# Optimization experiments

Measured on AMD Instinct MI355X. Metric: run time of the kernel, lower is better.

Reference implementation:

```python
import jax, jax.numpy as jnp
import numpy as np

D_MODEL = 768
NUM_HEADS = 12
D_K = D_MODEL // NUM_HEADS


def setup_inputs() -> dict:
    key = jax.random.key(0)
    ks = jax.random.split(key, 7)
    B, S = 4, 2048
    query = jax.random.normal(ks[0], (B, S, D_MODEL), dtype=jnp.float32)
    key_t = jax.random.normal(ks[1], (B, S, D_MODEL), dtype=jnp.float32)
    value = jax.random.normal(ks[2], (B, S, D_MODEL), dtype=jnp.float32)
    lim = 1.0 / np.sqrt(D_MODEL)
    Wq = jax.random.uniform(ks[3], (D_MODEL, D_MODEL), jnp.float32, -lim, lim)  # torch Linear weight [out,in]
    bq = jax.random.uniform(ks[4], (D_MODEL,), jnp.float32, -lim, lim)
    Wo = jax.random.uniform(ks[5], (D_MODEL, D_MODEL), jnp.float32, -lim, lim)
    bo = jax.random.uniform(ks[6], (D_MODEL,), jnp.float32, -lim, lim)
    return {"query": query, "key": key_t, "value": value,
            "Wq": Wq, "bq": bq, "Wo": Wo, "bo": bo}


def _proj_heads(x, W, b):
    # x: [B,S,D] -> [B,H,S,d_k]; torch Linear: x @ W.T + b
    B, S, _ = x.shape
    y = x @ W.T + b
    return y.reshape(B, S, NUM_HEADS, D_K).transpose(0, 2, 1, 3)


def reference(query, key, value, Wq, bq, Wo, bo):
    # Faithful to source: linear_q is used for q, k AND v (source bug).
    q = _proj_heads(query, Wq, bq)
    k = _proj_heads(key, Wq, bq)
    v = _proj_heads(value, Wq, bq)
    scale = 1.0 / jnp.sqrt(jnp.asarray(D_K, q.dtype))
    scores = jnp.einsum('bhqd,bhkd->bhqk', q, k) * scale  # [B,H,S,S]
    attn = jax.nn.softmax(scores, axis=-1)
    out = jnp.einsum('bhqk,bhkd->bhqd', attn, v)  # [B,H,S,d_k]
    B, H, S, dk = out.shape
    out = out.transpose(0, 2, 1, 3).reshape(B, S, H * dk)
    return out @ Wo.T + bo
```

## Files before the change

### kernel.cpp

```cpp
#include <hip/hip_runtime.h>
#include <math.h>

typedef _Float16 f16x8 __attribute__((ext_vector_type(8)));
typedef _Float16 f16x4 __attribute__((ext_vector_type(4)));
typedef float    f32x4 __attribute__((ext_vector_type(4)));
typedef unsigned short us4 __attribute__((ext_vector_type(4)));
typedef unsigned int u32;
typedef unsigned int u32x4 __attribute__((ext_vector_type(4)));

constexpr int DM = 768, NH = 12, DK = 64, SEQ = 2048, BB = 4;
constexpr int MROWS = BB * SEQ;
constexpr size_t XELE = (size_t)MROWS * DM;
constexpr size_t WELE = (size_t)DM * DM;

constexpr size_t OFF_X16  = 0;
constexpr size_t OFF_W16  = 3 * XELE;
constexpr size_t OFF_WO16 = OFF_W16 + WELE;
constexpr size_t OFF_QKV  = OFF_WO16 + WELE;
constexpr size_t OFF_ATT  = OFF_QKV + 3 * XELE;
constexpr size_t TOT_CVT  = OFF_QKV;


constexpr float QSCALE = 0.125f * 1.44269504f;
constexpr float MSEED = -8.0f;

__device__ __forceinline__ void gload16(const _Float16* g, _Float16* l) {
    __builtin_amdgcn_global_load_lds(
        (const __attribute__((address_space(1))) unsigned int*)g,
        (__attribute__((address_space(3))) unsigned int*)l, 16, 0, 0);
}

__device__ __forceinline__ uint2 pack4(float a, float b, float c, float d) {
    uint2 r;
    r.x = __builtin_bit_cast(u32, __builtin_amdgcn_cvt_pkrtz(a, b));
    r.y = __builtin_bit_cast(u32, __builtin_amdgcn_cvt_pkrtz(c, d));
    return r;
}

__global__ __launch_bounds__(256) void cvt_kernel(
    const float* __restrict__ q, const float* __restrict__ k,
    const float* __restrict__ v, const float* __restrict__ wq,
    const float* __restrict__ wo, _Float16* __restrict__ dst)
{
    const size_t i = ((size_t)blockIdx.x * 256 + threadIdx.x) * 4;
    if (i >= TOT_CVT) return;
    const float* src; size_t base;
    if      (i < XELE)            { src = q;  base = 0; }
    else if (i < 2 * XELE)        { src = k;  base = XELE; }
    else if (i < 3 * XELE)        { src = v;  base = 2 * XELE; }
    else if (i < OFF_WO16)        { src = wq; base = OFF_W16; }
    else                          { src = wo; base = OFF_WO16; }
    const float4 f = *(const float4*)(src + (i - base));
    _Float16 h4[4] = {(_Float16)f.x, (_Float16)f.y, (_Float16)f.z, (_Float16)f.w};
    *(us4*)(dst + i) = *(us4*)h4;
}

template <int MODE>
__global__ __launch_bounds__(256) void mfma_gemm(
    const _Float16* __restrict__ Xbase, const _Float16* __restrict__ Wmat,
    const float* __restrict__ bias, void* __restrict__ Yout)
{
    __shared__ _Float16 smem[(MODE == 0) ? 128 * 136 : 16384];

    const int bid = blockIdx.x;
    const int xs  = bid & 7;
    const int rr  = bid >> 3;
    const int m_blk = ((rr & 7) << 3) | xs;
    const int tt  = rr >> 3;
    const int n_blk = (MODE == 0) ? (tt % 6) : tt;
    const int z     = (MODE == 0) ? (tt / 6) : 0;

    const int tid  = threadIdx.x;
    const int w    = tid >> 6, lane = tid & 63;
    const int cl   = lane & 15;
    const int g    = lane >> 4;
    const int m0   = m_blk * 128, n0 = n_blk * 128;
    const _Float16* X = Xbase + (size_t)z * XELE;

    const int wr = w >> 1, wc = w & 1;
    const int lrow = lane >> 2;
    const int lcol = (lane & 3) * 8;

    f32x4 acc[4][4] = {};

    constexpr int NK = DM / 32;
#pragma unroll
    for (int t = 0; t < 2; ++t) {
        const int c = w + t * 4;
        gload16(X    + (size_t)(m0 + c * 16 + lrow) * DM + lcol, &smem[c * 512]);
        gload16(Wmat + (size_t)(n0 + c * 16 + lrow) * DM + lcol, &smem[4096 + c * 512]);
    }

    int cur = 0;
    for (int ki = 0; ki < NK; ++ki) {
        __syncthreads();
        if (ki + 1 < NK) {
            const int kn = (ki + 1) * 32;
            _Float16* dst = &smem[(cur ^ 1) * 8192];
#pragma unroll
            for (int t = 0; t < 2; ++t) {
                const int c = w + t * 4;
                gload16(X    + (size_t)(m0 + c * 16 + lrow) * DM + kn + lcol, &dst[c * 512]);
                gload16(Wmat + (size_t)(n0 + c * 16 + lrow) * DM + kn + lcol, &dst[4096 + c * 512]);
            }
        }
        const _Float16* As = &smem[cur * 8192];
        const _Float16* Bs = As + 4096;

        f16x8 a[4], bfr[4];
#pragma unroll
        for (int mt = 0; mt < 4; ++mt)
            a[mt] = *(const f16x8*)&As[(wr * 64 + mt * 16 + cl) * 32 + g * 8];
#pragma unroll
        for (int nt = 0; nt < 4; ++nt)
            bfr[nt] = *(const f16x8*)&Bs[(wc * 64 + nt * 16 + cl) * 32 + g * 8];
#pragma unroll
        for (int mt = 0; mt < 4; ++mt)
#pragma unroll
            for (int nt = 0; nt < 4; ++nt)
                acc[mt][nt] = __builtin_amdgcn_mfma_f32_16x16x32_f16(
                    a[mt], bfr[nt], acc[mt][nt], 0, 0, 0);
        cur ^= 1;
    }

    if (MODE == 1) {
#pragma unroll
        for (int nt = 0; nt < 4; ++nt) {
            const int col = n0 + wc * 64 + nt * 16 + cl;
            const float bv = bias[col];
#pragma unroll
            for (int mt = 0; mt < 4; ++mt)
#pragma unroll
                for (int r = 0; r < 4; ++r) {
                    const int row = m0 + wr * 64 + mt * 16 + g * 4 + r;
                    ((float*)Yout)[(size_t)row * DM + col] = acc[mt][nt][r] + bv;
                }
        }
        return;
    }

    __syncthreads();
    const float sc = (z == 0) ? QSCALE : 1.0f;
#pragma unroll
    for (int nt = 0; nt < 4; ++nt) {
        const int col = wc * 64 + nt * 16 + cl;
        const float bv = bias[n0 + col];
#pragma unroll
        for (int mt = 0; mt < 4; ++mt)
#pragma unroll
            for (int r = 0; r < 4; ++r) {
                const int row = wr * 64 + mt * 16 + g * 4 + r;
                const _Float16 hv = (_Float16)((acc[mt][nt][r] + bv) * sc);
                if (z == 2) smem[col * 136 + row] = hv;
                else        smem[row * 136 + col] = hv;
            }
    }
    __syncthreads();

    _Float16* Yz = (_Float16*)Yout + (size_t)z * XELE;
#pragma unroll
    for (int it = 0; it < 8; ++it) {
        const int idx = tid + it * 256;
        const int row = idx >> 4;
        const int grp = idx & 15;
        const f16x8 vv = *(const f16x8*)&smem[row * 136 + grp * 8];
        if (z == 2) {
            const int f  = n0 + row, hh = f >> 6, d = f & 63;
            const int gm = m0 + grp * 8;
            const int bb = gm >> 11, s = gm & (SEQ - 1);
            const int ssw = (s & ~63) | ((((s >> 3) & 7) ^ (d & 7)) << 3);
            *(f16x8*)&Yz[(((size_t)bb * NH + hh) * DK + d) * SEQ + ssw] = vv;
        } else {
            const int gm = m0 + row;
            const int bb = gm >> 11, s = gm & (SEQ - 1);
            const int n  = n0 + grp * 8, hh = n >> 6, d0 = n & 63;
            const int dsw = ((((d0 >> 3) ^ (s & 7)) & 7) << 3);
            *(f16x8*)&Yz[(((size_t)bb * NH + hh) * SEQ + s) * DK + dsw] = vv;
        }
    }
}

__global__ __launch_bounds__(256) void flash4(
    const _Float16* __restrict__ qkv, _Float16* __restrict__ attno)
{
    __shared__ _Float16 KsB[2 * 64 * 64];
    __shared__ _Float16 VtB[2 * 64 * 64];

    const int bid = blockIdx.x;
    const int xs  = bid & 7;
    const int rr  = bid >> 3;
    const int p   = (rr % 6) * 8 + xs;
    const int qtb = rr / 6;
    const int h   = p % NH, b = p / NH;
    const int q0  = qtb * 128;

    const int tid = threadIdx.x;
    const int w = tid >> 6, lane = tid & 63;
    const int cl = lane & 15, g = lane >> 4;
    const int swz = cl & 7;

    const size_t headoff = ((size_t)b * NH + h) * SEQ * DK;
    const _Float16* Qg = qkv + headoff;
    const _Float16* Kg = qkv + XELE + headoff;
    const _Float16* Vg = qkv + 2 * XELE + headoff;

    const int ldr = lane >> 3, ldc = (lane & 7) * 8;

#pragma unroll
    for (int t = 0; t < 2; ++t) {
        const int c = w * 2 + t;
        gload16(Kg + (size_t)(c * 8 + ldr) * DK + ldc, &KsB[c * 512]);
        gload16(Vg + (size_t)(c * 8 + ldr) * SEQ + ldc, &VtB[c * 512]);
    }

    f16x8 qf[2][2];
#pragma unroll
    for (int qt = 0; qt < 2; ++qt)
#pragma unroll
        for (int ks = 0; ks < 2; ++ks)
            qf[qt][ks] = *(const f16x8*)(
                Qg + (size_t)(q0 + w * 32 + qt * 16 + cl) * DK
                   + (((ks * 4 + g) ^ swz) << 3));

    float l_run[2] = {0.f, 0.f};
    f32x4 acc[2][4] = {};

    int cur = 0;
    for (int j0 = 0; j0 < SEQ; j0 += 64) {
        __syncthreads();
        if (j0 + 64 < SEQ) {
            const int jn = j0 + 64;
            _Float16* Kd = &KsB[(cur ^ 1) * 4096];
            _Float16* Vd = &VtB[(cur ^ 1) * 4096];
#pragma unroll
            for (int t = 0; t < 2; ++t) {
                const int c = w * 2 + t;
                gload16(Kg + (size_t)(jn + c * 8 + ldr) * DK + ldc, &Kd[c * 512]);
                gload16(Vg + (size_t)(c * 8 + ldr) * SEQ + jn + ldc, &Vd[c * 512]);
            }
        }
        const _Float16* Ks = &KsB[cur * 4096];
        const _Float16* Vt = &VtB[cur * 4096];

        f16x8 kf[4][2];
#pragma unroll
        for (int kt = 0; kt < 4; ++kt)
#pragma unroll
            for (int ks = 0; ks < 2; ++ks)
                kf[kt][ks] = *(const f16x8*)&Ks[(kt * 16 + cl) * 64
                                                + (((ks * 4 + g) ^ swz) << 3)];

        uint2 pk[2][4];
#pragma unroll
        for (int qt = 0; qt < 2; ++qt) {
            float ps = 0.f;
#pragma unroll
            for (int kt = 0; kt < 4; ++kt) {
                f32x4 s = {MSEED, MSEED, MSEED, MSEED};
#pragma unroll
                for (int ks = 0; ks < 2; ++ks)
                    s = __builtin_amdgcn_mfma_f32_16x16x32_f16(
                        kf[kt][ks], qf[qt][ks], s, 0, 0, 0);
                const float p0 = __builtin_amdgcn_exp2f(s[0]);
                const float p1 = __builtin_amdgcn_exp2f(s[1]);
                const float p2 = __builtin_amdgcn_exp2f(s[2]);
                const float p3 = __builtin_amdgcn_exp2f(s[3]);
                ps += (p0 + p1) + (p2 + p3);
                pk[qt][kt] = pack4(p0, p1, p2, p3);
            }
            l_run[qt] += ps;
        }

        f16x8 pf[2][2];
#pragma unroll
        for (int qt = 0; qt < 2; ++qt)
#pragma unroll
            for (int ks = 0; ks < 2; ++ks) {
                u32 a0 = pk[qt][2 * ks].x, b0 = pk[qt][2 * ks + 1].x;
                u32 a1 = pk[qt][2 * ks].y, b1 = pk[qt][2 * ks + 1].y;
                {
                    auto r = __builtin_amdgcn_permlane32_swap(a0, b0, false, false);
                    a0 = r[0]; b0 = r[1];
                }
                {
                    auto r = __builtin_amdgcn_permlane16_swap(a0, b0, false, false);
                    a0 = r[0]; b0 = r[1];
                }
                {
                    auto r = __builtin_amdgcn_permlane32_swap(a1, b1, false, false);
                    a1 = r[0]; b1 = r[1];
                }
                {
                    auto r = __builtin_amdgcn_permlane16_swap(a1, b1, false, false);
                    a1 = r[0]; b1 = r[1];
                }
                u32x4 wds = {a0, a1, b0, b1};
                pf[qt][ks] = __builtin_bit_cast(f16x8, wds);
            }

        f16x8 vf[4][2];
#pragma unroll
        for (int dt = 0; dt < 4; ++dt)
#pragma unroll
            for (int ks = 0; ks < 2; ++ks)
                vf[dt][ks] = *(const f16x8*)&Vt[(dt * 16 + cl) * 64
                                                + (((ks * 4 + g) ^ swz) << 3)];
#pragma unroll
        for (int qt = 0; qt < 2; ++qt)
#pragma unroll
            for (int ks = 0; ks < 2; ++ks)
#pragma unroll
                for (int dt = 0; dt < 4; ++dt)
                    acc[qt][dt] = __builtin_amdgcn_mfma_f32_16x16x32_f16(
                        vf[dt][ks], pf[qt][ks], acc[qt][dt], 0, 0, 0);
        cur ^= 1;
    }

#pragma unroll
    for (int qt = 0; qt < 2; ++qt) {
        float l = l_run[qt];
        l += __shfl_xor(l, 16);
        l += __shfl_xor(l, 32);
        const float inv = 1.0f / l;
        const int q = q0 + w * 32 + qt * 16 + cl;
#pragma unroll
        for (int dt = 0; dt < 4; ++dt) {
            uint2 pk2 = pack4(acc[qt][dt][0] * inv, acc[qt][dt][1] * inv,
                              acc[qt][dt][2] * inv, acc[qt][dt][3] * inv);
            *(uint2*)&attno[((size_t)b * SEQ + q) * DM + h * DK + dt * 16 + g * 4] = pk2;
        }
    }
}

extern "C" void kernel_launch(void* const* d_in, const int* in_sizes, int n_in,
                              void* d_out, int out_size, void* d_ws, size_t ws_size,
                              hipStream_t stream) {
    const float* q  = (const float*)d_in[0];
    const float* k  = (const float*)d_in[1];
    const float* v  = (const float*)d_in[2];
    const float* Wq = (const float*)d_in[3];
    const float* bq = (const float*)d_in[4];
    const float* Wo = (const float*)d_in[5];
    const float* bo = (const float*)d_in[6];

    _Float16* ws16  = (_Float16*)d_ws;
    _Float16* x16   = ws16 + OFF_X16;
    _Float16* w16   = ws16 + OFF_W16;
    _Float16* wo16  = ws16 + OFF_WO16;
    _Float16* qkv16 = ws16 + OFF_QKV;
    _Float16* att16 = ws16 + OFF_ATT;

    cvt_kernel<<<(int)(TOT_CVT / 1024), 256, 0, stream>>>(q, k, v, Wq, Wo, ws16);

    mfma_gemm<0><<<1152, 256, 0, stream>>>(x16, w16, bq, qkv16);

    flash4<<<768, 256, 0, stream>>>(qkv16, att16);

    mfma_gemm<1><<<384, 256, 0, stream>>>(att16, wo16, bo, (float*)d_out);
}
```

Before: 255.3 us.

## Load K and V fragments directly from global memory, dropping LDS double buffering

The flash attention kernel no longer stages K and V tiles through double-buffered shared memory with async global-to-LDS loads and per-iteration barriers. Each wave now reads its MFMA fragments straight from global memory, which already uses the swizzled layout, and the loop is unrolled by two. This removes the __syncthreads and LDS traffic. In exchange, every one of the four waves fetches the same K/V data separately through the L1/L2 caches, and global load latency is no longer hidden by an explicit prefetch.

```diff
diff --git a/kernel.cpp b/kernel.cpp
--- a/kernel.cpp
+++ b/kernel.cpp
@@ -183,9 +183,6 @@
 __global__ __launch_bounds__(256) void flash4(
     const _Float16* __restrict__ qkv, _Float16* __restrict__ attno)
 {
-    __shared__ _Float16 KsB[2 * 64 * 64];
-    __shared__ _Float16 VtB[2 * 64 * 64];
-
     const int bid = blockIdx.x;
     const int xs  = bid & 7;
     const int rr  = bid >> 3;
@@ -204,15 +201,6 @@
     const _Float16* Kg = qkv + XELE + headoff;
     const _Float16* Vg = qkv + 2 * XELE + headoff;
 
-    const int ldr = lane >> 3, ldc = (lane & 7) * 8;
-
-#pragma unroll
-    for (int t = 0; t < 2; ++t) {
-        const int c = w * 2 + t;
-        gload16(Kg + (size_t)(c * 8 + ldr) * DK + ldc, &KsB[c * 512]);
-        gload16(Vg + (size_t)(c * 8 + ldr) * SEQ + ldc, &VtB[c * 512]);
-    }
-
     f16x8 qf[2][2];
 #pragma unroll
     for (int qt = 0; qt < 2; ++qt)
@@ -225,30 +213,16 @@
     float l_run[2] = {0.f, 0.f};
     f32x4 acc[2][4] = {};
 
-    int cur = 0;
+#pragma unroll 2
     for (int j0 = 0; j0 < SEQ; j0 += 64) {
-        __syncthreads();
-        if (j0 + 64 < SEQ) {
-            const int jn = j0 + 64;
-            _Float16* Kd = &KsB[(cur ^ 1) * 4096];
-            _Float16* Vd = &VtB[(cur ^ 1) * 4096];
-#pragma unroll
-            for (int t = 0; t < 2; ++t) {
-                const int c = w * 2 + t;
-                gload16(Kg + (size_t)(jn + c * 8 + ldr) * DK + ldc, &Kd[c * 512]);
-                gload16(Vg + (size_t)(c * 8 + ldr) * SEQ + jn + ldc, &Vd[c * 512]);
-            }
-        }
-        const _Float16* Ks = &KsB[cur * 4096];
-        const _Float16* Vt = &VtB[cur * 4096];
-
         f16x8 kf[4][2];
 #pragma unroll
         for (int kt = 0; kt < 4; ++kt)
 #pragma unroll
             for (int ks = 0; ks < 2; ++ks)
-                kf[kt][ks] = *(const f16x8*)&Ks[(kt * 16 + cl) * 64
-                                                + (((ks * 4 + g) ^ swz) << 3)];
+                kf[kt][ks] = *(const f16x8*)(
+                    Kg + (size_t)(j0 + kt * 16 + cl) * DK
+                       + (((ks * 4 + g) ^ swz) << 3));
 
         uint2 pk[2][4];
 #pragma unroll
@@ -303,8 +277,10 @@
         for (int dt = 0; dt < 4; ++dt)
 #pragma unroll
             for (int ks = 0; ks < 2; ++ks)
-                vf[dt][ks] = *(const f16x8*)&Vt[(dt * 16 + cl) * 64
-                                                + (((ks * 4 + g) ^ swz) << 3)];
+                vf[dt][ks] = *(const f16x8*)(
+                    Vg + (size_t)(dt * 16 + cl) * SEQ + j0
+                       + (((ks * 4 + g) ^ swz) << 3));
+
 #pragma unroll
         for (int qt = 0; qt < 2; ++qt)
 #pragma unroll
@@ -313,7 +289,6 @@
                 for (int dt = 0; dt < 4; ++dt)
                     acc[qt][dt] = __builtin_amdgcn_mfma_f32_16x16x32_f16(
                         vf[dt][ks], pf[qt][ks], acc[qt][dt], 0, 0, 0);
-        cur ^= 1;
     }
 
 #pragma unroll
```

New measurement: 321.9 us. +26.1%, slower.
